# Performance work log

Hardware: AMD Instinct MI355X
Metric: run time of the kernel (lower is better)

The kernel has to match this reference:

```python
import jax, jax.numpy as jnp
import numpy as np

IN_C = 256
OUT_C = 256
KS = 3
PAD = 1
EPS = 1e-5
BLOCK_SIZE = 256  # largest power of 2 dividing IN_C
NUM_BLOCKS = IN_C // BLOCK_SIZE


def golay_sequence(n):
    pow2 = 1
    while pow2 < n:
        pow2 *= 2
    a = np.array([1.0], dtype=np.float32)
    b = np.array([1.0], dtype=np.float32)
    while len(a) < pow2:
        a, b = np.concatenate([a, b]), np.concatenate([a, -b])
    return a[:n]


def fwht(x):
    """Unnormalized fast Walsh-Hadamard transform over the last axis (Sylvester order)."""
    base = x.shape[:-1]
    n = x.shape[-1]
    h = 1
    while h < n:
        y = x.reshape(base + (n // (2 * h), 2, h))
        a, c = y[..., 0, :], y[..., 1, :]
        x = jnp.stack([a + c, a - c], axis=-2).reshape(base + (n,))
        h *= 2
    return x


def setup_inputs() -> dict:
    key = jax.random.key(0)
    k1, k2, k3 = jax.random.split(key, 3)
    x = jax.random.normal(k1, (32, IN_C, 56, 56), dtype=jnp.float32)
    fan_in = IN_C * KS * KS
    W = jax.random.normal(k2, (OUT_C, IN_C, KS, KS), dtype=jnp.float32) / np.sqrt(fan_in)
    b = jax.random.normal(k3, (OUT_C,), dtype=jnp.float32) * 0.01
    rms_w = jnp.ones((IN_C,), dtype=jnp.float32)
    return {"x": x, "W": W, "b": b, "rms_w": rms_w}


def reference(x, W, b, rms_w):
    n, c, h, w = x.shape
    golay = jnp.asarray(golay_sequence(c)).reshape(1, c, 1, 1)
    x = x * golay                                    # Golay elementwise multiply
    x = jnp.transpose(x, (0, 2, 3, 1))               # NCHW -> NHWC
    x = x.reshape(n, h, w, NUM_BLOCKS, BLOCK_SIZE)
    x = fwht(x)                                      # blockwise Hadamard butterfly
    x = x.reshape(n, h, w, c)
    # RMSNorm over channel dim
    x = x * jax.lax.rsqrt(jnp.mean(x * x, axis=-1, keepdims=True) + EPS) * rms_w
    x = jnp.transpose(x, (0, 3, 1, 2))               # NHWC -> NCHW
    out = jax.lax.conv_general_dilated(
        x, W, window_strides=(1, 1), padding=((PAD, PAD), (PAD, PAD)),
        dimension_numbers=("NCHW", "OIHW", "NCHW"))
    return out + b[None, :, None, None]
```

## Files before the change

kernel.cpp:

```cpp
#include <hip/hip_runtime.h>
#include <hip/hip_bf16.h>

typedef short v8s __attribute__((ext_vector_type(8)));
typedef float v4f __attribute__((ext_vector_type(4)));
typedef float v16f __attribute__((ext_vector_type(16)));
typedef unsigned short u16;

#define PROW 58
#define PCOL 64

static constexpr size_t A_CC_STRIDE = (size_t)32 * PROW * PCOL * 32;
static constexpr size_t A_BYTES     = 8 * A_CC_STRIDE * 2;
static constexpr size_t WB_ELEMS    = (size_t)9 * 8 * 256 * 32;

__device__ __forceinline__ void gl2lds16(const void* gptr, void* lptr) {
  auto g = (const __attribute__((address_space(1))) unsigned int*)gptr;
  auto l = (__attribute__((address_space(3))) unsigned int*)lptr;
  __builtin_amdgcn_global_load_lds(g, l, 16, 0, 0);
}

__device__ __forceinline__ u16 f2bf(float f) {
  __hip_bfloat16 h = __float2bfloat16(f);
  union { __hip_bfloat16 b; u16 u; } cv; cv.b = h; return cv.u;
}

struct alignas(16) HgTab {
  u16 v[16 * 8 * 64 * 8];
  constexpr HgTab() : v{} {
    for (int ks = 0; ks < 16; ks++)
      for (int nt = 0; nt < 8; nt++)
        for (int l = 0; l < 64; l++)
          for (int j = 0; j < 8; j++) {
            int c  = ks * 16 + ((l >> 5) << 3) + j;
            int cp = (nt << 5) + (l & 31);
            int s  = (__builtin_popcount((unsigned)(c & cp)) +
                      __builtin_popcount((unsigned)(c & (c >> 1)))) & 1;
            v[(((ks << 3) + nt) << 9) + (l << 3) + j] = (u16)(s ? 0xBF80 : 0x3F80);
          }
  }
};
static_assert(sizeof(HgTab) == 131072, "HgTab size");
__device__ const HgTab HG{};

__global__ __launch_bounds__(256, 4) void fwht_kernel(
    const float* __restrict__ x, const float* __restrict__ rms_w,
    u16* __restrict__ A)
{
  __shared__ __align__(16) float xs[4][2][16][64];
  __shared__ float ssbuf[2][64];

  const int tid = threadIdx.x;
  const int y = blockIdx.x;
  const int n = blockIdx.y;

  const int lane = tid & 63;
  const int wv   = tid >> 6;
  const int mt   = wv & 1;
  const int nh   = wv >> 1;
  const int l31  = lane & 31;
  const int h    = lane >> 5;

  const int pos  = mt * 32 + l31;
  const int posl = pos > 55 ? 55 : pos;

  const float* xrow = x + (size_t)n * 802816 + (size_t)y * 56;
  const int rr = lane >> 4;
  int c4 = (lane & 15) * 4; if (c4 > 52) c4 = 52;

  float* db0 = &xs[wv][0][0][0];
  float* db1 = &xs[wv][1][0][0];

  auto stage = [&](int ks, float* db) {
    const float* sb = xrow + (size_t)(ks * 16 + rr) * 3136 + c4;
    #pragma unroll
    for (int k = 0; k < 4; k++)
      gl2lds16(sb + (size_t)(k * 4) * 3136, db + k * 256 + lane * 4);
  };

  v16f acc[4];
  #pragma unroll
  for (int nt = 0; nt < 4; nt++)
    #pragma unroll
    for (int e = 0; e < 16; e++)
      acc[nt][e] = 0.0f;

  stage(0, db0);

  #pragma unroll
  for (int ks = 0; ks < 16; ks++) {
    float* cb = (ks & 1) ? db1 : db0;
    float* nb = (ks & 1) ? db0 : db1;

    v8s bfr[4];
    #pragma unroll
    for (int nt = 0; nt < 4; nt++)
      bfr[nt] = *(const v8s*)(HG.v + ((size_t)(((ks * 8) + nh * 4 + nt) * 64 + lane)) * 8);
    __builtin_amdgcn_sched_barrier(0);

    if (ks < 15) stage(ks + 1, nb);
    __builtin_amdgcn_sched_barrier(0);

    asm volatile("s_waitcnt vmcnt(4)" ::: "memory");
    __builtin_amdgcn_sched_barrier(0);

    v8s ah, al;
    #pragma unroll
    for (int j = 0; j < 8; j++) {
      float v = cb[(h * 8 + j) * 64 + posl];
      unsigned u  = __float_as_uint(v);
      unsigned hu = u & 0xFFFF0000u;
      float r = v - __uint_as_float(hu);
      ah[j] = (short)(hu >> 16);
      al[j] = (short)f2bf(r);
    }
    #pragma unroll
    for (int nt = 0; nt < 4; nt++) {
      acc[nt] = __builtin_amdgcn_mfma_f32_32x32x16_bf16(ah, bfr[nt], acc[nt], 0, 0, 0);
      acc[nt] = __builtin_amdgcn_mfma_f32_32x32x16_bf16(al, bfr[nt], acc[nt], 0, 0, 0);
    }
  }

  #pragma unroll
  for (int g = 0; g < 16; g++) {
    float s = acc[0][g] * acc[0][g] + acc[1][g] * acc[1][g]
            + acc[2][g] * acc[2][g] + acc[3][g] * acc[3][g];
    #pragma unroll
    for (int m = 1; m <= 16; m <<= 1) s += __shfl_xor(s, m, 64);
    if (l31 == 0)
      ssbuf[nh][mt * 32 + (g & 3) + 8 * (g >> 2) + 4 * h] = s;
  }
  __syncthreads();

  float rwv[4];
  #pragma unroll
  for (int nt = 0; nt < 4; nt++)
    rwv[nt] = rms_w[nh * 128 + nt * 32 + l31];

  const int jj  = lane & 7;
  const int icq = l31 >> 3;

  #pragma unroll
  for (int g = 0; g < 16; g++) {
    const int rg   = (g & 3) + 8 * (g >> 2) + 4 * h;
    const int posg = mt * 32 + rg;
    float ssum = ssbuf[0][posg] + ssbuf[1][posg];
    float sc = rsqrtf(ssum * (1.0f / 256.0f) + 1e-5f);
    if (posg < 56) {
      const int col = posg + 1;
      const size_t rowoff = ((size_t)icq * 64 + col) * 8 + jj;
      #pragma unroll
      for (int nt = 0; nt < 4; nt++) {
        const int cc = nh * 4 + nt;
        size_t go = (((size_t)cc * 32 + n) * PROW + (y + 1)) * 2048 + rowoff;
        A[go] = f2bf(acc[nt][g] * sc * rwv[nt]);
      }
    }
  }

  {
    const v8s z = {0,0,0,0,0,0,0,0};
    int cc = tid >> 5;
    int s  = tid & 31;
    int q  = s >> 3, cidx = s & 7;
    int col = (cidx == 0) ? 0 : (56 + cidx);
    size_t rb = (((size_t)cc * 32 + n) * PROW + (y + 1)) * 2048;
    *(v8s*)(A + rb + ((size_t)q * 64 + col) * 8) = z;
  }
  if (y == 0 || y == 55) {
    const v8s z = {0,0,0,0,0,0,0,0};
    const int r = (y == 0) ? 0 : 57;
    #pragma unroll
    for (int i = 0; i < 8; i++) {
      int c = tid + 256 * i;
      int cc = c >> 8, rem = c & 255;
      size_t go = (((size_t)cc * 32 + n) * PROW + r) * 2048 + rem * 8;
      *(v8s*)(A + go) = z;
    }
  }
}

__global__ __launch_bounds__(256) void wconv_kernel(
    const float* __restrict__ Wf, u16* __restrict__ Wb)
{
  int t = blockIdx.x * 256 + threadIdx.x;
  int kk = t >> 16;
  int cc = (t >> 13) & 7;
  int r  = t & 8191;
  int ocb = r >> 12;
  int q   = (r >> 10) & 3;
  int ocl = (r >> 3) & 127;
  int j   = r & 7;
  int oc = ocb * 128 + ocl;
  int ic = cc * 32 + q * 8 + j;
  int ky = kk / 3, kx = kk - ky * 3;
  float w = Wf[((oc * 256 + ic) * 3 + ky) * 3 + kx];
  Wb[t] = f2bf(w);
}

__global__ __launch_bounds__(256, 4) void conv_kernel(
    const u16* __restrict__ A, const u16* __restrict__ Wb,
    const float* __restrict__ bias, float* __restrict__ out)
{
  __shared__ __align__(16) u16 As[4 * 2048];
  __shared__ __align__(16) u16 Bs[3 * 4096];

  const int tid  = threadIdx.x;
  const int lane = tid & 63;
  const int wv   = tid >> 6;
  const int wm   = wv & 1;
  const int wn   = wv >> 1;
  const int m31  = lane & 31;
  const int kh8  = lane >> 5;

  const int ocb = blockIdx.x;
  const int y0  = blockIdx.y * 2;
  const int n   = blockIdx.z;

  const u16* gA = A + ((size_t)n * PROW + y0) * 2048;

  v16f acc[2][2];
  #pragma unroll
  for (int i = 0; i < 2; i++)
    #pragma unroll
    for (int j = 0; j < 2; j++)
      #pragma unroll
      for (int e = 0; e < 16; e++)
        acc[i][j][e] = 0.0f;

  int ub[2][2];
  #pragma unroll
  for (int nf = 0; nf < 2; nf++)
    #pragma unroll
    for (int kh = 0; kh < 2; kh++) {
      int ocl = wn * 64 + nf * 32 + m31;
      int q = kh * 2 + kh8;
      ub[nf][kh] = (q * 128 + ocl) * 8;
    }

  auto stageA = [&](int cc) {
    const u16* g = gA + (size_t)cc * A_CC_STRIDE + tid * 8;
    u16* d = As + tid * 8;
    #pragma unroll
    for (int k = 0; k < 4; k++)
      gl2lds16(g + k * 2048, d + k * 2048);
  };
  auto stageB = [&](int cc, int ky) {
    #pragma unroll
    for (int kx = 0; kx < 3; kx++) {
      const int kk = ky * 3 + kx;
      const u16* g = Wb + ((kk * 8 + cc) * 8192 + ocb * 4096) + tid * 8;
      u16* d = Bs + kx * 4096 + tid * 8;
      gl2lds16(g, d);
      gl2lds16(g + 2048, d + 2048);
    }
  };

  for (int cc = 0; cc < 8; cc++) {
    __syncthreads();
    stageA(cc);
    stageB(cc, 0);
    __syncthreads();
    #pragma unroll
    for (int ky = 0; ky < 3; ky++) {
      #pragma unroll
      for (int kx = 0; kx < 3; kx++) {
        v8s af[2][2];
        #pragma unroll
        for (int mf = 0; mf < 2; mf++)
          #pragma unroll
          for (int kh = 0; kh < 2; kh++) {
            int col = mf * 32 + m31 + kx;
            col = col > 63 ? 63 : col;
            int q = kh * 2 + kh8;
            int ua = ((wm + ky) * 4 + q) * 512 + col * 8;
            af[mf][kh] = *(const v8s*)(As + ua);
          }
        v8s bf[2][2];
        const u16* bsb = Bs + kx * 4096;
        #pragma unroll
        for (int nf = 0; nf < 2; nf++)
          #pragma unroll
          for (int kh = 0; kh < 2; kh++)
            bf[nf][kh] = *(const v8s*)(bsb + ub[nf][kh]);
        #pragma unroll
        for (int mf = 0; mf < 2; mf++)
          #pragma unroll
          for (int nf = 0; nf < 2; nf++) {
            acc[mf][nf] = __builtin_amdgcn_mfma_f32_32x32x16_bf16(af[mf][0], bf[nf][0], acc[mf][nf], 0, 0, 0);
            acc[mf][nf] = __builtin_amdgcn_mfma_f32_32x32x16_bf16(af[mf][1], bf[nf][1], acc[mf][nf], 0, 0, 0);
          }
      }
      if (ky < 2) {
        __syncthreads();
        stageB(cc, ky + 1);
        __syncthreads();
      }
    }
  }

  const int yrow = y0 + wm;
  #pragma unroll
  for (int nf = 0; nf < 2; nf++) {
    const int oc = ocb * 128 + wn * 64 + nf * 32 + m31;
    const float bb = bias[oc];
    float* orow = out + ((size_t)(n * 256 + oc) * 56 + yrow) * 56;
    #pragma unroll
    for (int mf = 0; mf < 2; mf++) {
      #pragma unroll
      for (int g = 0; g < 4; g++) {
        const int x0 = mf * 32 + 8 * g + 4 * kh8;
        if (x0 < 56) {
          v4f val = { acc[mf][nf][4*g+0] + bb, acc[mf][nf][4*g+1] + bb,
                      acc[mf][nf][4*g+2] + bb, acc[mf][nf][4*g+3] + bb };
          *(v4f*)(orow + x0) = val;
        }
      }
    }
  }
}

extern "C" void kernel_launch(void* const* d_in, const int* in_sizes, int n_in,
                              void* d_out, int out_size, void* d_ws, size_t ws_size,
                              hipStream_t stream)
{
  const float* x     = (const float*)d_in[0];
  const float* Wf    = (const float*)d_in[1];
  const float* bias  = (const float*)d_in[2];
  const float* rms_w = (const float*)d_in[3];
  float* out = (float*)d_out;

  if (ws_size < A_BYTES + WB_ELEMS * 2) return;

  u16* Abf = (u16*)d_ws;
  u16* Wb  = (u16*)((char*)d_ws + A_BYTES);

  fwht_kernel<<<dim3(56, 32), 256, 0, stream>>>(x, rms_w, Abf);
  wconv_kernel<<<dim3((int)(WB_ELEMS / 256)), 256, 0, stream>>>(Wf, Wb);
  conv_kernel<<<dim3(2, 28, 32), 256, 0, stream>>>(Abf, Wb, bias, out);
}
```

Before: 352.2 us.

## Double-buffer conv LDS stages and deepen FWHT prefetch pipeline

The conv kernel now double-buffers both the activation and weight tiles in LDS. It prefetches the next (cc, ky) phase with async global-to-LDS loads while computing the current one, uses vmcnt waits instead of paired syncthreads, and raises MFMA priority. The FWHT kernel moves to a 4-slot ring buffer shared across waves, prefetching 3 stages ahead and loading the Hadamard table one stage early. The cost is more LDS per block and a lower occupancy hint for the conv kernel (2 blocks instead of 4), which reduces latency hiding from extra waves.

```diff
diff --git a/kernel.cpp b/kernel.cpp
--- a/kernel.cpp
+++ b/kernel.cpp
@@ -23,6 +23,8 @@
   __hip_bfloat16 h = __float2bfloat16(f);
   union { __hip_bfloat16 b; u16 u; } cv; cv.b = h; return cv.u;
 }
+
+#define WAITVM(K) __builtin_amdgcn_s_waitcnt(0xF70 | (K))
 
 struct alignas(16) HgTab {
   u16 v[16 * 8 * 64 * 8];
@@ -46,7 +48,7 @@
     const float* __restrict__ x, const float* __restrict__ rms_w,
     u16* __restrict__ A)
 {
-  __shared__ __align__(16) float xs[4][2][16][64];
+  __shared__ __align__(16) float xs4[4][16][64];
   __shared__ float ssbuf[2][64];
 
   const int tid = threadIdx.x;
@@ -64,18 +66,15 @@
   const int posl = pos > 55 ? 55 : pos;
 
   const float* xrow = x + (size_t)n * 802816 + (size_t)y * 56;
-  const int rr = lane >> 4;
+  const int rr4 = lane >> 4;
   int c4 = (lane & 15) * 4; if (c4 > 52) c4 = 52;
 
-  float* db0 = &xs[wv][0][0][0];
-  float* db1 = &xs[wv][1][0][0];
-
-  auto stage = [&](int ks, float* db) {
-    const float* sb = xrow + (size_t)(ks * 16 + rr) * 3136 + c4;
-    #pragma unroll
-    for (int k = 0; k < 4; k++)
-      gl2lds16(sb + (size_t)(k * 4) * 3136, db + k * 256 + lane * 4);
-  };
+#define FSTG(KS) gl2lds16(xrow + (size_t)((KS) * 16 + wv * 4 + rr4) * 3136 + c4, \
+                          &xs4[(KS) & 3][wv * 4 + rr4][(lane & 15) * 4])
+
+  v8s bfr[2][4];
+#define LOADB(KS, BK) { _Pragma("unroll") for (int nt = 0; nt < 4; nt++) \
+    bfr[BK][nt] = *(const v8s*)(HG.v + ((size_t)((((KS) * 8) + nh * 4 + nt) * 64 + lane)) * 8); }
 
   v16f acc[4];
   #pragma unroll
@@ -84,41 +83,37 @@
     for (int e = 0; e < 16; e++)
       acc[nt][e] = 0.0f;
 
-  stage(0, db0);
-
-  #pragma unroll
-  for (int ks = 0; ks < 16; ks++) {
-    float* cb = (ks & 1) ? db1 : db0;
-    float* nb = (ks & 1) ? db0 : db1;
-
-    v8s bfr[4];
-    #pragma unroll
-    for (int nt = 0; nt < 4; nt++)
-      bfr[nt] = *(const v8s*)(HG.v + ((size_t)(((ks * 8) + nh * 4 + nt) * 64 + lane)) * 8);
-    __builtin_amdgcn_sched_barrier(0);
-
-    if (ks < 15) stage(ks + 1, nb);
-    __builtin_amdgcn_sched_barrier(0);
-
-    asm volatile("s_waitcnt vmcnt(4)" ::: "memory");
-    __builtin_amdgcn_sched_barrier(0);
-
-    v8s ah, al;
-    #pragma unroll
-    for (int j = 0; j < 8; j++) {
-      float v = cb[(h * 8 + j) * 64 + posl];
-      unsigned u  = __float_as_uint(v);
-      unsigned hu = u & 0xFFFF0000u;
-      float r = v - __uint_as_float(hu);
-      ah[j] = (short)(hu >> 16);
-      al[j] = (short)f2bf(r);
-    }
-    #pragma unroll
-    for (int nt = 0; nt < 4; nt++) {
-      acc[nt] = __builtin_amdgcn_mfma_f32_32x32x16_bf16(ah, bfr[nt], acc[nt], 0, 0, 0);
-      acc[nt] = __builtin_amdgcn_mfma_f32_32x32x16_bf16(al, bfr[nt], acc[nt], 0, 0, 0);
-    }
-  }
+  FSTG(0);
+  LOADB(0, 0)
+  FSTG(1);
+  FSTG(2);
+
+#define FCOMP(S) { const float* cb = &xs4[(S) & 3][0][0]; v8s ah, al; \
+    _Pragma("unroll") for (int j = 0; j < 8; j++) { \
+      float v = cb[(h * 8 + j) * 64 + posl]; \
+      unsigned u = __float_as_uint(v); \
+      unsigned hu = u & 0xFFFF0000u; \
+      float r = v - __uint_as_float(hu); \
+      ah[j] = (short)(hu >> 16); \
+      al[j] = (short)f2bf(r); } \
+    _Pragma("unroll") for (int nt = 0; nt < 4; nt++) { \
+      acc[nt] = __builtin_amdgcn_mfma_f32_32x32x16_bf16(ah, bfr[(S) & 1][nt], acc[nt], 0, 0, 0); \
+      acc[nt] = __builtin_amdgcn_mfma_f32_32x32x16_bf16(al, bfr[(S) & 1][nt], acc[nt], 0, 0, 0); } }
+
+#define FSTEP(S, KV) { \
+    if ((S) < 15) LOADB((S) + 1, ((S) + 1) & 1) \
+    __builtin_amdgcn_sched_barrier(0); \
+    WAITVM(KV); \
+    __builtin_amdgcn_sched_barrier(0); \
+    __builtin_amdgcn_s_barrier(); \
+    if ((S) + 3 <= 15) { FSTG((S) + 3); } \
+    __builtin_amdgcn_sched_barrier(0); \
+    FCOMP(S) }
+
+  FSTEP(0, 6)  FSTEP(1, 5)  FSTEP(2, 5)  FSTEP(3, 5)
+  FSTEP(4, 5)  FSTEP(5, 5)  FSTEP(6, 5)  FSTEP(7, 5)
+  FSTEP(8, 5)  FSTEP(9, 5)  FSTEP(10, 5) FSTEP(11, 5)
+  FSTEP(12, 5) FSTEP(13, 5) FSTEP(14, 4) FSTEP(15, 0)
 
   #pragma unroll
   for (int g = 0; g < 16; g++) {
@@ -177,6 +172,10 @@
       *(v8s*)(A + go) = z;
     }
   }
+#undef FSTG
+#undef LOADB
+#undef FCOMP
+#undef FSTEP
 }
 
 __global__ __launch_bounds__(256) void wconv_kernel(
@@ -197,12 +196,12 @@
   Wb[t] = f2bf(w);
 }
 
-__global__ __launch_bounds__(256, 4) void conv_kernel(
+__global__ __launch_bounds__(256, 2) void conv_kernel(
     const u16* __restrict__ A, const u16* __restrict__ Wb,
     const float* __restrict__ bias, float* __restrict__ out)
 {
-  __shared__ __align__(16) u16 As[4 * 2048];
-  __shared__ __align__(16) u16 Bs[3 * 4096];
+  __shared__ __align__(16) u16 As2[2][8192];
+  __shared__ __align__(16) u16 Bs2[2][12288];
 
   const int tid  = threadIdx.x;
   const int lane = tid & 63;
@@ -237,66 +236,62 @@
       ub[nf][kh] = (q * 128 + ocl) * 8;
     }
 
-  auto stageA = [&](int cc) {
-    const u16* g = gA + (size_t)cc * A_CC_STRIDE + tid * 8;
-    u16* d = As + tid * 8;
-    #pragma unroll
-    for (int k = 0; k < 4; k++)
-      gl2lds16(g + k * 2048, d + k * 2048);
-  };
-  auto stageB = [&](int cc, int ky) {
-    #pragma unroll
-    for (int kx = 0; kx < 3; kx++) {
-      const int kk = ky * 3 + kx;
-      const u16* g = Wb + ((kk * 8 + cc) * 8192 + ocb * 4096) + tid * 8;
-      u16* d = Bs + kx * 4096 + tid * 8;
-      gl2lds16(g, d);
-      gl2lds16(g + 2048, d + 2048);
-    }
-  };
-
-  for (int cc = 0; cc < 8; cc++) {
-    __syncthreads();
-    stageA(cc);
-    stageB(cc, 0);
-    __syncthreads();
-    #pragma unroll
-    for (int ky = 0; ky < 3; ky++) {
-      #pragma unroll
-      for (int kx = 0; kx < 3; kx++) {
-        v8s af[2][2];
-        #pragma unroll
-        for (int mf = 0; mf < 2; mf++)
-          #pragma unroll
-          for (int kh = 0; kh < 2; kh++) {
-            int col = mf * 32 + m31 + kx;
-            col = col > 63 ? 63 : col;
-            int q = kh * 2 + kh8;
-            int ua = ((wm + ky) * 4 + q) * 512 + col * 8;
-            af[mf][kh] = *(const v8s*)(As + ua);
-          }
-        v8s bf[2][2];
-        const u16* bsb = Bs + kx * 4096;
-        #pragma unroll
-        for (int nf = 0; nf < 2; nf++)
-          #pragma unroll
-          for (int kh = 0; kh < 2; kh++)
-            bf[nf][kh] = *(const v8s*)(bsb + ub[nf][kh]);
-        #pragma unroll
-        for (int mf = 0; mf < 2; mf++)
-          #pragma unroll
-          for (int nf = 0; nf < 2; nf++) {
-            acc[mf][nf] = __builtin_amdgcn_mfma_f32_32x32x16_bf16(af[mf][0], bf[nf][0], acc[mf][nf], 0, 0, 0);
-            acc[mf][nf] = __builtin_amdgcn_mfma_f32_32x32x16_bf16(af[mf][1], bf[nf][1], acc[mf][nf], 0, 0, 0);
-          }
-      }
-      if (ky < 2) {
-        __syncthreads();
-        stageB(cc, ky + 1);
-        __syncthreads();
-      }
-    }
-  }
+#define STAGE_A(CCV) { const u16* g = gA + (size_t)(CCV) * A_CC_STRIDE + tid * 8; \
+    u16* d = &As2[(CCV) & 1][0] + tid * 8; \
+    _Pragma("unroll") for (int k = 0; k < 4; k++) gl2lds16(g + k * 2048, d + k * 2048); }
+
+#define STAGE_B(CCV, KYV, BUF) { _Pragma("unroll") for (int kx = 0; kx < 3; kx++) { \
+    const u16* g = Wb + ((((KYV) * 3 + kx) * 8 + (CCV)) * 8192 + ocb * 4096) + tid * 8; \
+    u16* d = &Bs2[BUF][kx * 4096] + tid * 8; \
+    gl2lds16(g, d); gl2lds16(g + 2048, d + 2048); } }
+
+#define CONV_PHASE(P) { \
+    if ((P) < 23) { \
+      STAGE_B(((P) + 1) / 3, ((P) + 1) % 3, ((P) + 1) & 1) \
+      if (((P) + 1) % 3 == 0) STAGE_A((((P) + 1) / 3) & 1 ? (((P) + 1) / 3) : (((P) + 1) / 3)) \
+    } \
+    __builtin_amdgcn_sched_barrier(0); \
+    WAITVM((P) == 23 ? 0 : (((P) + 1) % 3 == 0 ? 10 : 6)); \
+    __builtin_amdgcn_sched_barrier(0); \
+    __builtin_amdgcn_s_barrier(); \
+    { const u16* asb = &As2[((P) / 3) & 1][0]; \
+      const u16* bsb0 = &Bs2[(P) & 1][0]; \
+      _Pragma("unroll") for (int kx = 0; kx < 3; kx++) { \
+        v8s af[2][2]; \
+        _Pragma("unroll") for (int mf = 0; mf < 2; mf++) \
+          _Pragma("unroll") for (int kh = 0; kh < 2; kh++) { \
+            int col = mf * 32 + m31 + kx; \
+            col = col > 63 ? 63 : col; \
+            int q = kh * 2 + kh8; \
+            int ua = ((wm + ((P) % 3)) * 4 + q) * 512 + col * 8; \
+            af[mf][kh] = *(const v8s*)(asb + ua); } \
+        v8s bf[2][2]; const u16* bsb = bsb0 + kx * 4096; \
+        _Pragma("unroll") for (int nf = 0; nf < 2; nf++) \
+          _Pragma("unroll") for (int kh = 0; kh < 2; kh++) \
+            bf[nf][kh] = *(const v8s*)(bsb + ub[nf][kh]); \
+        __builtin_amdgcn_s_setprio(1); \
+        _Pragma("unroll") for (int mf = 0; mf < 2; mf++) \
+          _Pragma("unroll") for (int nf = 0; nf < 2; nf++) { \
+            acc[mf][nf] = __builtin_amdgcn_mfma_f32_32x32x16_bf16(af[mf][0], bf[nf][0], acc[mf][nf], 0, 0, 0); \
+            acc[mf][nf] = __builtin_amdgcn_mfma_f32_32x32x16_bf16(af[mf][1], bf[nf][1], acc[mf][nf], 0, 0, 0); } \
+        __builtin_amdgcn_s_setprio(0); \
+      } \
+    } \
+    __builtin_amdgcn_s_barrier(); }
+
+  STAGE_B(0, 0, 0)
+  STAGE_A(0)
+
+  CONV_PHASE(0)  CONV_PHASE(1)  CONV_PHASE(2)  CONV_PHASE(3)
+  CONV_PHASE(4)  CONV_PHASE(5)  CONV_PHASE(6)  CONV_PHASE(7)
+  CONV_PHASE(8)  CONV_PHASE(9)  CONV_PHASE(10) CONV_PHASE(11)
+  CONV_PHASE(12) CONV_PHASE(13) CONV_PHASE(14) CONV_PHASE(15)
+  CONV_PHASE(16) CONV_PHASE(17) CONV_PHASE(18) CONV_PHASE(19)
+  CONV_PHASE(20) CONV_PHASE(21) CONV_PHASE(22) CONV_PHASE(23)
+
+#undef STAGE_A
+#undef STAGE_B
+#undef CONV_PHASE
 
   const int yrow = y0 + wm;
   #pragma unroll
```

Measured after the change: 335.2 us. 1.05x faster.
